# Performance work log

Measured on AMD Instinct MI355X. Metric: run time of the kernel, lower is better.

## Reference

```python
import jax, jax.numpy as jnp
import numpy as np

EPS_F = 1e-12
M, N = 64, 4096  # feature dim m, num nodes n


def setup_inputs() -> dict:
    key = jax.random.key(0)
    k1, k2, k3, k4 = jax.random.split(key, 4)
    # X: (m, n) node features transposed, as in the repo (features.t())
    X = jax.random.normal(k1, (M, N), dtype=jnp.float32)
    # F: (m, m) parameter, xavier_uniform init
    bound = float(np.sqrt(6.0 / (M + M)))
    F = jax.random.uniform(k2, (M, M), minval=-bound, maxval=bound, dtype=jnp.float32)
    # Q_S: (n, n) orthogonal eigenvector matrix of the (symmetric, normalized) adjacency
    A = jax.random.normal(k3, (N, N), dtype=jnp.float32)
    Q_S, _ = jnp.linalg.qr(A)
    Q_S = Q_S.astype(jnp.float32)
    # Lambda_S: (n, 1) eigenvalues of normalized adjacency, inside (-1, 1)
    Lambda_S = jnp.sort(
        jax.random.uniform(k4, (N, 1), minval=-0.95, maxval=0.95, dtype=jnp.float32), axis=0
    )
    gamma = jnp.asarray(0.8, dtype=jnp.float32)
    return {"X": X, "F": F, "Q_S": Q_S, "Lambda_S": Lambda_S, "gamma": gamma}


def reference(X, F, Q_S, Lambda_S, gamma):
    # g(F) = F^T F / (||F^T F||_F + eps)  -- Frobenius-normalized Gram matrix
    FF = F.T @ F                                   # (m, m)
    G_F = FF / (jnp.linalg.norm(FF) + EPS_F)       # (m, m), symmetric PSD, ||.||_F ~ 1
    # spectral decomposition of g(F)
    Lambda_F, Q_F = jnp.linalg.eigh(G_F)           # (m,), (m, m)
    # closed-form equilibrium of Z = gamma * g(F) Z S^T + X in the joint eigenbasis
    D = 1.0 / (1.0 - gamma * Lambda_F[:, None] * Lambda_S.reshape(1, -1))  # (m, n)
    Z = Q_F @ (D * (Q_F.T @ X @ Q_S)) @ Q_S.T      # (m, n)
    return Z
```

## Files before the change

kernel.cpp:

```cpp
#include <hip/hip_runtime.h>
#include <math.h>


typedef short short8 __attribute__((ext_vector_type(8)));
typedef float floatx16 __attribute__((ext_vector_type(16)));

#define KSPLIT 8
#define KCHUNK 512
constexpr int Mdim = 64;
constexpr int Ndim = 4096;

__device__ inline ushort f2bf(float f) {
    uint u = __float_as_uint(f);
    u += 0x7fff + ((u >> 16) & 1);
    return (ushort)(u >> 16);
}
__device__ inline float bf2f(ushort h) { return __uint_as_float(((uint)h) << 16); }

__device__ inline floatx16 mfma_bf16(short8 a, short8 b, floatx16 c) {
    return __builtin_amdgcn_mfma_f32_32x32x16_bf16(a, b, c, 0, 0, 0);
}


__global__ __launch_bounds__(256) void prep_kernel(const float* __restrict__ F,
                                                   float* __restrict__ Gout) {
    __shared__ float Fraw[64 * 65];
    __shared__ ushort Ph[64 * 64];
    __shared__ ushort Pl[64 * 64];
    __shared__ float red[256];
    const int t = threadIdx.x;
    const int l = t & 63, w = t >> 6;
    const int tm = w & 1, tn = w >> 1;
    const int am = tm * 32 + (l & 31);
    const int bn = tn * 32 + (l & 31);
    const int lk = l >> 5;

    for (int s = 0; s < 4; ++s) {
        int e = t + 256 * s;
        int r = e >> 4, q = (e & 15) * 4;
        float4 v = *(const float4*)&F[r * 64 + q];
        float fa[4] = {v.x, v.y, v.z, v.w};
        for (int i = 0; i < 4; ++i) Fraw[r * 65 + q + i] = fa[i];
    }
    __syncthreads();
    {
        int c = t >> 2, kbase = (t & 3) * 16;
        ushort hh[16], ll[16];
        for (int kk = 0; kk < 16; ++kk) {
            float v = Fraw[(kbase + kk) * 65 + c];
            ushort h = f2bf(v);
            hh[kk] = h;
            ll[kk] = f2bf(v - bf2f(h));
        }
        for (int g = 0; g < 2; ++g) {
            int gk = (kbase >> 3) + g;
            int idx = c * 64 + ((gk ^ (c & 7)) * 8);
            for (int u = 0; u < 8; ++u) { Ph[idx + u] = hh[8 * g + u]; Pl[idx + u] = ll[8 * g + u]; }
        }
    }
    __syncthreads();
    floatx16 acc;
    for (int i = 0; i < 16; ++i) acc[i] = 0.f;
    for (int s16 = 0; s16 < 4; ++s16) {
        int gk = 2 * s16 + lk;
        int ai = am * 64 + ((gk ^ (am & 7)) * 8);
        int bi = bn * 64 + ((gk ^ (bn & 7)) * 8);
        short8 ah = *(const short8*)&Ph[ai];
        short8 al = *(const short8*)&Pl[ai];
        short8 bh = *(const short8*)&Ph[bi];
        short8 bl = *(const short8*)&Pl[bi];
        acc = mfma_bf16(ah, bh, acc);
        acc = mfma_bf16(al, bh, acc);
        acc = mfma_bf16(ah, bl, acc);
    }
    float ss = 0.f;
    for (int r = 0; r < 16; ++r) ss += acc[r] * acc[r];
    red[t] = ss;
    __syncthreads();
    for (int off = 128; off > 0; off >>= 1) {
        if (t < off) red[t] += red[t + off];
        __syncthreads();
    }
    const float inv = 1.0f / (sqrtf(red[0]) + 1e-12f);
    for (int r = 0; r < 16; ++r) {
        int row = (r & 3) + 8 * (r >> 2) + 4 * lk + tm * 32;
        int col = tn * 32 + (l & 31);
        float v = acc[r] * inv;
        Gout[row * 64 + col] = v;
        ushort h = f2bf(v);
        int idx = row * 64 + (((col >> 3) ^ (row & 7)) * 8 + (col & 7));
        Ph[idx] = h;
        Pl[idx] = f2bf(v - bf2f(h));
    }
    for (int j = 1; j < 5; ++j) {
        __syncthreads();
        floatx16 a2;
        for (int i = 0; i < 16; ++i) a2[i] = 0.f;
        for (int s16 = 0; s16 < 4; ++s16) {
            int gk = 2 * s16 + lk;
            int ai = am * 64 + ((gk ^ (am & 7)) * 8);
            int bi = bn * 64 + ((gk ^ (bn & 7)) * 8);
            short8 ah = *(const short8*)&Ph[ai];
            short8 al = *(const short8*)&Pl[ai];
            short8 bh = *(const short8*)&Ph[bi];
            short8 bl = *(const short8*)&Pl[bi];
            a2 = mfma_bf16(ah, bh, a2);
            a2 = mfma_bf16(al, bh, a2);
            a2 = mfma_bf16(ah, bl, a2);
        }
        __syncthreads();
        for (int r = 0; r < 16; ++r) {
            int row = (r & 3) + 8 * (r >> 2) + 4 * lk + tm * 32;
            int col = tn * 32 + (l & 31);
            float v = a2[r];
            Gout[j * 4096 + row * 64 + col] = v;
            ushort h = f2bf(v);
            int idx = row * 64 + (((col >> 3) ^ (row & 7)) * 8 + (col & 7));
            Ph[idx] = h;
            Pl[idx] = f2bf(v - bf2f(h));
        }
    }
}

template <bool TB>
__global__ __launch_bounds__(256) void gemm_kernel(const float* __restrict__ A,
                                                   const float* __restrict__ Bm,
                                                   float* __restrict__ C) {
    __shared__ ushort Ah[64 * 64], Al[64 * 64], Bh[64 * 64], Bl[64 * 64];
    const int t = threadIdx.x;
    const int n0 = blockIdx.x * 64;
    const int kb = blockIdx.y * KCHUNK;
    const int l = t & 63, w = t >> 6;
    const int tm = w & 1, tn = w >> 1;
    const int am = tm * 32 + (l & 31);
    const int bn = tn * 32 + (l & 31);
    const int lk = l >> 5;
    const int sr = t >> 2, sj = t & 3;
    const int nq = t & 15, kr2 = 2 * (t >> 4);

    floatx16 acc;
    for (int i = 0; i < 16; ++i) acc[i] = 0.f;

    for (int step = 0; step < KCHUNK / 64; ++step) {
        const int k0 = kb + step * 64;
        float4 av[4], bv[4], bva[2], bvb[2];
        for (int s = 0; s < 4; ++s)
            av[s] = *(const float4*)&A[sr * 4096 + k0 + 4 * sj + 16 * s];
        if (TB) {
            for (int s = 0; s < 4; ++s)
                bv[s] = *(const float4*)&Bm[(size_t)(n0 + sr) * 4096 + k0 + 4 * sj + 16 * s];
        } else {
            for (int s = 0; s < 2; ++s) {
                bva[s] = *(const float4*)&Bm[(size_t)(k0 + kr2 + 32 * s) * 4096 + n0 + 4 * nq];
                bvb[s] = *(const float4*)&Bm[(size_t)(k0 + kr2 + 1 + 32 * s) * 4096 + n0 + 4 * nq];
            }
        }
        __syncthreads();
        for (int s = 0; s < 4; ++s) {
            int off = 4 * sj + 16 * s;
            int idx = sr * 64 + (((off >> 3) ^ (sr & 7)) * 8 + (off & 7));
            float fa[4] = {av[s].x, av[s].y, av[s].z, av[s].w};
            ushort4 h4, l4;
            ushort* hp = (ushort*)&h4; ushort* lp = (ushort*)&l4;
            for (int i = 0; i < 4; ++i) {
                ushort h = f2bf(fa[i]);
                hp[i] = h; lp[i] = f2bf(fa[i] - bf2f(h));
            }
            *(ushort4*)&Ah[idx] = h4;
            *(ushort4*)&Al[idx] = l4;
        }
        if (TB) {
            for (int s = 0; s < 4; ++s) {
                int off = 4 * sj + 16 * s;
                int idx = sr * 64 + (((off >> 3) ^ (sr & 7)) * 8 + (off & 7));
                float fb[4] = {bv[s].x, bv[s].y, bv[s].z, bv[s].w};
                ushort4 h4, l4;
                ushort* hp = (ushort*)&h4; ushort* lp = (ushort*)&l4;
                for (int i = 0; i < 4; ++i) {
                    ushort h = f2bf(fb[i]);
                    hp[i] = h; lp[i] = f2bf(fb[i] - bf2f(h));
                }
                *(ushort4*)&Bh[idx] = h4;
                *(ushort4*)&Bl[idx] = l4;
            }
        } else {
            for (int s = 0; s < 2; ++s) {
                int k = kr2 + 32 * s;
                float fa[4] = {bva[s].x, bva[s].y, bva[s].z, bva[s].w};
                float fb[4] = {bvb[s].x, bvb[s].y, bvb[s].z, bvb[s].w};
                for (int i = 0; i < 4; ++i) {
                    int n = 4 * nq + i;
                    int idx = n * 64 + (((k >> 3) ^ (n & 7)) * 8 + (k & 7));
                    ushort2 hp2, lp2;
                    hp2.x = f2bf(fa[i]); hp2.y = f2bf(fb[i]);
                    lp2.x = f2bf(fa[i] - bf2f(hp2.x));
                    lp2.y = f2bf(fb[i] - bf2f(hp2.y));
                    *(ushort2*)&Bh[idx] = hp2;
                    *(ushort2*)&Bl[idx] = lp2;
                }
            }
        }
        __syncthreads();
#pragma unroll
        for (int s16 = 0; s16 < 4; ++s16) {
            int gk = 2 * s16 + lk;
            int ai = am * 64 + ((gk ^ (am & 7)) * 8);
            int bi = bn * 64 + ((gk ^ (bn & 7)) * 8);
            short8 ah = *(const short8*)&Ah[ai];
            short8 al = *(const short8*)&Al[ai];
            short8 bh = *(const short8*)&Bh[bi];
            short8 bl = *(const short8*)&Bl[bi];
            acc = mfma_bf16(ah, bh, acc);
            acc = mfma_bf16(al, bh, acc);
            acc = mfma_bf16(ah, bl, acc);
        }
    }
    const int colg = n0 + tn * 32 + (l & 31);
#pragma unroll
    for (int r = 0; r < 16; ++r) {
        int row = (r & 3) + 8 * (r >> 2) + 4 * lk + tm * 32;
        atomicAdd(&C[row * 4096 + colg], acc[r]);
    }
}

__global__ __launch_bounds__(256) void solve_kernel(const float* __restrict__ W,
                                                    const float* __restrict__ Gp,
                                                    const float* __restrict__ lam,
                                                    const float* __restrict__ gammap,
                                                    float* __restrict__ Y) {
    __shared__ float Gs[64][68];
    __shared__ float T[64][17];
    const int t = threadIdx.x;
    const int c0 = blockIdx.x * 16;
    for (int e = t; e < 1024; e += 256)
        T[e >> 4][e & 15] = W[(e >> 4) * 4096 + c0 + (e & 15)];
    const int tx = t & 15;
    const int r4 = (t >> 4) * 4;
    const float a = gammap[0] * lam[c0 + tx];
    float s = a;
    for (int j = 0; j < 5; ++j) {
        __syncthreads();
        for (int e = t; e < 4096; e += 256) Gs[e >> 6][e & 63] = Gp[j * 4096 + e];
        __syncthreads();
        float u0 = 0.f, u1 = 0.f, u2 = 0.f, u3 = 0.f;
#pragma unroll 8
        for (int k = 0; k < 64; ++k) {
            const float tv = T[k][tx];
            const float4 g = *(const float4*)&Gs[k][r4];
            u0 += g.x * tv; u1 += g.y * tv; u2 += g.z * tv; u3 += g.w * tv;
        }
        __syncthreads();
        T[r4 + 0][tx] += s * u0;
        T[r4 + 1][tx] += s * u1;
        T[r4 + 2][tx] += s * u2;
        T[r4 + 3][tx] += s * u3;
        s = s * s;
    }
    __syncthreads();
    for (int e = t; e < 1024; e += 256)
        Y[(e >> 4) * 4096 + c0 + (e & 15)] = T[e >> 4][e & 15];
}

extern "C" void kernel_launch(void* const* d_in, const int* in_sizes, int n_in,
                              void* d_out, int out_size, void* d_ws, size_t ws_size,
                              hipStream_t stream) {
    const float* X     = (const float*)d_in[0];
    const float* F     = (const float*)d_in[1];
    const float* Qs    = (const float*)d_in[2];
    const float* lam   = (const float*)d_in[3];
    const float* gamma = (const float*)d_in[4];
    float* Z = (float*)d_out;

    float* W  = (float*)d_ws;
    float* Y  = W + Mdim * Ndim;
    float* Gp = Y + Mdim * Ndim;

    hipMemsetAsync(W, 0, Mdim * Ndim * sizeof(float), stream);
    hipMemsetAsync(Z, 0, Mdim * Ndim * sizeof(float), stream);

    prep_kernel<<<1, 256, 0, stream>>>(F, Gp);
    gemm_kernel<false><<<dim3(Ndim / 64, KSPLIT), 256, 0, stream>>>(X, Qs, W);
    solve_kernel<<<Ndim / 16, 256, 0, stream>>>(W, Gp, lam, gamma, Y);
    gemm_kernel<true><<<dim3(Ndim / 64, KSPLIT), 256, 0, stream>>>(Y, Qs, Z);
}
```

Before: 163.5 us.

## Replace atomic split-K with slab partials, fold prep into GEMM, drop memsets

Doubles the split-K factor, so each GEMM launches 1024 blocks over 256-wide K chunks. Each split now writes plain stores into its own partial slab instead of doing atomicAdd into one buffer. The partials are summed inside the solve kernel's load for the first GEMM and by a new reduce kernel for the second. The single-block prep work now runs as an extra block of the first GEMM launch through a shared-memory union, which removes a separate launch and both memsets. In exchange it uses a much larger workspace and adds extra global traffic to read back the 16 slabs.

```diff
diff --git a/kernel.cpp b/kernel.cpp
--- a/kernel.cpp
+++ b/kernel.cpp
@@ -5,10 +5,11 @@
 typedef short short8 __attribute__((ext_vector_type(8)));
 typedef float floatx16 __attribute__((ext_vector_type(16)));
 
-#define KSPLIT 8
-#define KCHUNK 512
+#define KSPLIT 16
+#define KCHUNK 256
 constexpr int Mdim = 64;
 constexpr int Ndim = 4096;
+constexpr int SLAB = Mdim * Ndim;
 
 __device__ inline ushort f2bf(float f) {
     uint u = __float_as_uint(f);
@@ -21,13 +22,11 @@
     return __builtin_amdgcn_mfma_f32_32x32x16_bf16(a, b, c, 0, 0, 0);
 }
 
-
-__global__ __launch_bounds__(256) void prep_kernel(const float* __restrict__ F,
-                                                   float* __restrict__ Gout) {
-    __shared__ float Fraw[64 * 65];
-    __shared__ ushort Ph[64 * 64];
-    __shared__ ushort Pl[64 * 64];
-    __shared__ float red[256];
+struct SharedGemm { ushort Ah[4096], Al[4096], Bh[4096], Bl[4096]; };
+struct SharedPrep { float Fraw[64 * 65]; ushort Ph[4096], Pl[4096]; float red[256]; };
+union SharedU { SharedGemm g; SharedPrep p; };
+
+__device__ void prep_body(SharedPrep& sp, const float* __restrict__ F, float* __restrict__ Gout) {
     const int t = threadIdx.x;
     const int l = t & 63, w = t >> 6;
     const int tm = w & 1, tn = w >> 1;
@@ -40,22 +39,25 @@
         int r = e >> 4, q = (e & 15) * 4;
         float4 v = *(const float4*)&F[r * 64 + q];
         float fa[4] = {v.x, v.y, v.z, v.w};
-        for (int i = 0; i < 4; ++i) Fraw[r * 65 + q + i] = fa[i];
+        for (int i = 0; i < 4; ++i) sp.Fraw[r * 65 + q + i] = fa[i];
     }
     __syncthreads();
     {
         int c = t >> 2, kbase = (t & 3) * 16;
         ushort hh[16], ll[16];
+#pragma unroll
         for (int kk = 0; kk < 16; ++kk) {
-            float v = Fraw[(kbase + kk) * 65 + c];
+            float v = sp.Fraw[(kbase + kk) * 65 + c];
             ushort h = f2bf(v);
             hh[kk] = h;
             ll[kk] = f2bf(v - bf2f(h));
         }
+#pragma unroll
         for (int g = 0; g < 2; ++g) {
             int gk = (kbase >> 3) + g;
             int idx = c * 64 + ((gk ^ (c & 7)) * 8);
-            for (int u = 0; u < 8; ++u) { Ph[idx + u] = hh[8 * g + u]; Pl[idx + u] = ll[8 * g + u]; }
+#pragma unroll
+            for (int u = 0; u < 8; ++u) { sp.Ph[idx + u] = hh[8 * g + u]; sp.Pl[idx + u] = ll[8 * g + u]; }
         }
     }
     __syncthreads();
@@ -65,23 +67,23 @@
         int gk = 2 * s16 + lk;
         int ai = am * 64 + ((gk ^ (am & 7)) * 8);
         int bi = bn * 64 + ((gk ^ (bn & 7)) * 8);
-        short8 ah = *(const short8*)&Ph[ai];
-        short8 al = *(const short8*)&Pl[ai];
-        short8 bh = *(const short8*)&Ph[bi];
-        short8 bl = *(const short8*)&Pl[bi];
+        short8 ah = *(const short8*)&sp.Ph[ai];
+        short8 al = *(const short8*)&sp.Pl[ai];
+        short8 bh = *(const short8*)&sp.Ph[bi];
+        short8 bl = *(const short8*)&sp.Pl[bi];
         acc = mfma_bf16(ah, bh, acc);
         acc = mfma_bf16(al, bh, acc);
         acc = mfma_bf16(ah, bl, acc);
     }
     float ss = 0.f;
     for (int r = 0; r < 16; ++r) ss += acc[r] * acc[r];
-    red[t] = ss;
+    sp.red[t] = ss;
     __syncthreads();
     for (int off = 128; off > 0; off >>= 1) {
-        if (t < off) red[t] += red[t + off];
-        __syncthreads();
-    }
-    const float inv = 1.0f / (sqrtf(red[0]) + 1e-12f);
+        if (t < off) sp.red[t] += sp.red[t + off];
+        __syncthreads();
+    }
+    const float inv = 1.0f / (sqrtf(sp.red[0]) + 1e-12f);
     for (int r = 0; r < 16; ++r) {
         int row = (r & 3) + 8 * (r >> 2) + 4 * lk + tm * 32;
         int col = tn * 32 + (l & 31);
@@ -89,8 +91,8 @@
         Gout[row * 64 + col] = v;
         ushort h = f2bf(v);
         int idx = row * 64 + (((col >> 3) ^ (row & 7)) * 8 + (col & 7));
-        Ph[idx] = h;
-        Pl[idx] = f2bf(v - bf2f(h));
+        sp.Ph[idx] = h;
+        sp.Pl[idx] = f2bf(v - bf2f(h));
     }
     for (int j = 1; j < 5; ++j) {
         __syncthreads();
@@ -100,10 +102,10 @@
             int gk = 2 * s16 + lk;
             int ai = am * 64 + ((gk ^ (am & 7)) * 8);
             int bi = bn * 64 + ((gk ^ (bn & 7)) * 8);
-            short8 ah = *(const short8*)&Ph[ai];
-            short8 al = *(const short8*)&Pl[ai];
-            short8 bh = *(const short8*)&Ph[bi];
-            short8 bl = *(const short8*)&Pl[bi];
+            short8 ah = *(const short8*)&sp.Ph[ai];
+            short8 al = *(const short8*)&sp.Pl[ai];
+            short8 bh = *(const short8*)&sp.Ph[bi];
+            short8 bl = *(const short8*)&sp.Pl[bi];
             a2 = mfma_bf16(ah, bh, a2);
             a2 = mfma_bf16(al, bh, a2);
             a2 = mfma_bf16(ah, bl, a2);
@@ -116,20 +118,27 @@
             Gout[j * 4096 + row * 64 + col] = v;
             ushort h = f2bf(v);
             int idx = row * 64 + (((col >> 3) ^ (row & 7)) * 8 + (col & 7));
-            Ph[idx] = h;
-            Pl[idx] = f2bf(v - bf2f(h));
-        }
-    }
-}
-
-template <bool TB>
-__global__ __launch_bounds__(256) void gemm_kernel(const float* __restrict__ A,
-                                                   const float* __restrict__ Bm,
-                                                   float* __restrict__ C) {
-    __shared__ ushort Ah[64 * 64], Al[64 * 64], Bh[64 * 64], Bl[64 * 64];
+            sp.Ph[idx] = h;
+            sp.Pl[idx] = f2bf(v - bf2f(h));
+        }
+    }
+}
+
+template <bool TB, bool DOPREP>
+__global__ __launch_bounds__(256, 4) void gemm_kernel(const float* __restrict__ A,
+                                                      const float* __restrict__ Bm,
+                                                      float* __restrict__ C,
+                                                      const float* __restrict__ F,
+                                                      float* __restrict__ Gp) {
+    __shared__ SharedU sh;
+    const int bid = blockIdx.x;
+    if (DOPREP) {
+        if (bid == 0) { prep_body(sh.p, F, Gp); return; }
+    }
+    const int b = DOPREP ? bid - 1 : bid;
+    const int n0 = (b & 63) * 64;
+    const int kb = (b >> 6) * KCHUNK;
     const int t = threadIdx.x;
-    const int n0 = blockIdx.x * 64;
-    const int kb = blockIdx.y * KCHUNK;
     const int l = t & 63, w = t >> 6;
     const int tm = w & 1, tn = w >> 1;
     const int am = tm * 32 + (l & 31);
@@ -166,8 +175,8 @@
                 ushort h = f2bf(fa[i]);
                 hp[i] = h; lp[i] = f2bf(fa[i] - bf2f(h));
             }
-            *(ushort4*)&Ah[idx] = h4;
-            *(ushort4*)&Al[idx] = l4;
+            *(ushort4*)&sh.g.Ah[idx] = h4;
+            *(ushort4*)&sh.g.Al[idx] = l4;
         }
         if (TB) {
             for (int s = 0; s < 4; ++s) {
@@ -180,8 +189,8 @@
                     ushort h = f2bf(fb[i]);
                     hp[i] = h; lp[i] = f2bf(fb[i] - bf2f(h));
                 }
-                *(ushort4*)&Bh[idx] = h4;
-                *(ushort4*)&Bl[idx] = l4;
+                *(ushort4*)&sh.g.Bh[idx] = h4;
+                *(ushort4*)&sh.g.Bl[idx] = l4;
             }
         } else {
             for (int s = 0; s < 2; ++s) {
@@ -195,8 +204,8 @@
                     hp2.x = f2bf(fa[i]); hp2.y = f2bf(fb[i]);
                     lp2.x = f2bf(fa[i] - bf2f(hp2.x));
                     lp2.y = f2bf(fb[i] - bf2f(hp2.y));
-                    *(ushort2*)&Bh[idx] = hp2;
-                    *(ushort2*)&Bl[idx] = lp2;
+                    *(ushort2*)&sh.g.Bh[idx] = hp2;
+                    *(ushort2*)&sh.g.Bl[idx] = lp2;
                 }
             }
         }
@@ -206,20 +215,21 @@
             int gk = 2 * s16 + lk;
             int ai = am * 64 + ((gk ^ (am & 7)) * 8);
             int bi = bn * 64 + ((gk ^ (bn & 7)) * 8);
-            short8 ah = *(const short8*)&Ah[ai];
-            short8 al = *(const short8*)&Al[ai];
-            short8 bh = *(const short8*)&Bh[bi];
-            short8 bl = *(const short8*)&Bl[bi];
+            short8 ah = *(const short8*)&sh.g.Ah[ai];
+            short8 al = *(const short8*)&sh.g.Al[ai];
+            short8 bh = *(const short8*)&sh.g.Bh[bi];
+            short8 bl = *(const short8*)&sh.g.Bl[bi];
             acc = mfma_bf16(ah, bh, acc);
             acc = mfma_bf16(al, bh, acc);
             acc = mfma_bf16(ah, bl, acc);
         }
     }
+    float* Cslab = C + (size_t)(b >> 6) * SLAB;
     const int colg = n0 + tn * 32 + (l & 31);
 #pragma unroll
     for (int r = 0; r < 16; ++r) {
         int row = (r & 3) + 8 * (r >> 2) + 4 * lk + tm * 32;
-        atomicAdd(&C[row * 4096 + colg], acc[r]);
+        Cslab[row * 4096 + colg] = acc[r];
     }
 }
 
@@ -232,8 +242,13 @@
     __shared__ float T[64][17];
     const int t = threadIdx.x;
     const int c0 = blockIdx.x * 16;
-    for (int e = t; e < 1024; e += 256)
-        T[e >> 4][e & 15] = W[(e >> 4) * 4096 + c0 + (e & 15)];
+    for (int e = t; e < 1024; e += 256) {
+        const int r = e >> 4, c = c0 + (e & 15);
+        float s = 0.f;
+#pragma unroll
+        for (int bsl = 0; bsl < KSPLIT; ++bsl) s += W[bsl * SLAB + r * 4096 + c];
+        T[r][e & 15] = s;
+    }
     const int tx = t & 15;
     const int r4 = (t >> 4) * 4;
     const float a = gammap[0] * lam[c0 + tx];
@@ -259,6 +274,18 @@
     __syncthreads();
     for (int e = t; e < 1024; e += 256)
         Y[(e >> 4) * 4096 + c0 + (e & 15)] = T[e >> 4][e & 15];
+}
+
+__global__ __launch_bounds__(256) void reduce_kernel(const float* __restrict__ P,
+                                                     float* __restrict__ Z) {
+    const int i = blockIdx.x * 256 + threadIdx.x;
+    float4 a = {0.f, 0.f, 0.f, 0.f};
+#pragma unroll
+    for (int bsl = 0; bsl < KSPLIT; ++bsl) {
+        float4 v = *(const float4*)&P[(size_t)bsl * SLAB + i * 4];
+        a.x += v.x; a.y += v.y; a.z += v.z; a.w += v.w;
+    }
+    *(float4*)&Z[i * 4] = a;
 }
 
 extern "C" void kernel_launch(void* const* d_in, const int* in_sizes, int n_in,
@@ -271,15 +298,13 @@
     const float* gamma = (const float*)d_in[4];
     float* Z = (float*)d_out;
 
-    float* W  = (float*)d_ws;
-    float* Y  = W + Mdim * Ndim;
-    float* Gp = Y + Mdim * Ndim;
-
-    hipMemsetAsync(W, 0, Mdim * Ndim * sizeof(float), stream);
-    hipMemsetAsync(Z, 0, Mdim * Ndim * sizeof(float), stream);
-
-    prep_kernel<<<1, 256, 0, stream>>>(F, Gp);
-    gemm_kernel<false><<<dim3(Ndim / 64, KSPLIT), 256, 0, stream>>>(X, Qs, W);
-    solve_kernel<<<Ndim / 16, 256, 0, stream>>>(W, Gp, lam, gamma, Y);
-    gemm_kernel<true><<<dim3(Ndim / 64, KSPLIT), 256, 0, stream>>>(Y, Qs, Z);
-}
+    float* P1 = (float*)d_ws;
+    float* P2 = P1 + (size_t)KSPLIT * SLAB;
+    float* Gp = P2 + (size_t)KSPLIT * SLAB;
+    float* Y  = Gp + 5 * 4096;
+
+    gemm_kernel<false, true><<<64 * KSPLIT + 1, 256, 0, stream>>>(X, Qs, P1, F, Gp);
+    solve_kernel<<<Ndim / 16, 256, 0, stream>>>(P1, Gp, lam, gamma, Y);
+    gemm_kernel<true, false><<<64 * KSPLIT, 256, 0, stream>>>(Y, Qs, P2, nullptr, nullptr);
+    reduce_kernel<<<256, 256, 0, stream>>>(P2, Z);
+}
```

After: 170.3 us. +4.2%, slower.
